# Kernel tuning notes

Hardware: AMD Instinct MI355X
Metric: run time of the kernel (lower is better)

Reference implementation:

```python
import jax, jax.numpy as jnp
import numpy as np
from jax import lax

K = 35
PAD = K // 2  # 17

def _maxpool_same(x):
    # x: [B, H, W]; torch MaxPool2d pads with -inf, stride 1, same spatial size
    return lax.reduce_window(
        x, -jnp.inf, lax.max,
        window_dimensions=(1, K, K),
        window_strides=(1, 1, 1),
        padding=[(0, 0), (PAD, PAD), (PAD, PAD)],
    )

def setup_inputs() -> dict:
    key = jax.random.key(0)
    k1, k2 = jax.random.split(key)
    shape = (16, 3, 512, 512)
    restored = jax.random.uniform(k1, shape, dtype=jnp.float32)
    target = jax.random.uniform(k2, shape, dtype=jnp.float32)
    return {"restored": restored, "target": target}

def reference(restored, target):
    r = _maxpool_same(jnp.min(restored, axis=1))  # channel-min then 35x35 max
    t = _maxpool_same(jnp.min(target, axis=1))
    out = jnp.mean(jnp.abs(r - t))
    return jax.nn.sigmoid(out)
```

## Files before the change

### kernel.cpp

```cpp
#include <hip/hip_runtime.h>
#include <math.h>

#define WID 512
#define HEI 512
#define NB  16
#define HW  ((size_t)HEI * WID)
#define NEG_INF (-INFINITY)

__global__ __launch_bounds__(256) void hmax_kernel(
    const float* __restrict__ rin, const float* __restrict__ tin,
    float* __restrict__ ws)
{
    const int h = blockIdx.x;
    const int z = blockIdx.y;
    const int b = z & 15;
    const float* __restrict__ in = (z < NB) ? rin : tin;
    const float* __restrict__ p  = in + (size_t)b * 3 * HW + (size_t)h * WID;

    __shared__ float sm[548];
    __shared__ float gm[137];

    const int tid = threadIdx.x;

    for (int i = tid; i < 548; i += 256) {
        int w = i - 17;
        float v = NEG_INF;
        if (w >= 0 && w < WID) {
            float a0 = __builtin_nontemporal_load(p + w);
            float a1 = __builtin_nontemporal_load(p + HW + w);
            float a2 = __builtin_nontemporal_load(p + 2 * HW + w);
            v = fminf(fminf(a0, a1), a2);
        }
        sm[i] = v;
    }
    __syncthreads();

    for (int g = tid; g < 137; g += 256) {
        gm[g] = fmaxf(fmaxf(sm[4*g], sm[4*g+1]), fmaxf(sm[4*g+2], sm[4*g+3]));
    }
    __syncthreads();

    float* __restrict__ wp = ws + (size_t)z * HW + (size_t)h * WID;
    #pragma unroll
    for (int rep = 0; rep < 2; ++rep) {
        const int a  = tid + rep * 256;
        const int bb = a + 34;
        const int j0 = (a + 3) >> 2;
        float m = fmaxf(fmaxf(sm[a], sm[a+1]), sm[a+2]);
        m = fmaxf(m, fmaxf(fmaxf(sm[bb], sm[bb-1]), sm[bb-2]));
        #pragma unroll
        for (int j = 0; j < 8; ++j) m = fmaxf(m, gm[j0 + j]);
        wp[a] = m;
    }
}

__global__ __launch_bounds__(256) void vmax_kernel(
    const float* __restrict__ rh, const float* __restrict__ th,
    float* __restrict__ acc)
{
    __shared__ float sm[100][64];
    __shared__ float gm[25][64];
    __shared__ float red[256];

    const int tid = threadIdx.x;
    const int col = tid & 63;
    const int ty  = tid >> 6;
    const int w0  = blockIdx.x * 64;
    const int h0  = blockIdx.y * 64;
    const int b   = blockIdx.z;

    float rtv[16];
    float tsum = 0.0f;

    #pragma unroll
    for (int tensor = 0; tensor < 2; ++tensor) {
        const float* __restrict__ pb =
            ((tensor == 0) ? rh : th) + (size_t)b * HW;

        for (int i = tid; i < 100 * 64; i += 256) {
            int row = i >> 6;
            int c   = i & 63;
            int hh  = h0 - 17 + row;
            float v = NEG_INF;
            if (row < 98 && hh >= 0 && hh < HEI)
                v = pb[(size_t)hh * WID + w0 + c];
            sm[row][c] = v;
        }
        __syncthreads();

        for (int i = tid; i < 25 * 64; i += 256) {
            int g = i >> 6;
            int c = i & 63;
            gm[g][c] = fmaxf(fmaxf(sm[4*g][c], sm[4*g+1][c]),
                             fmaxf(sm[4*g+2][c], sm[4*g+3][c]));
        }
        __syncthreads();

        #pragma unroll
        for (int k = 0; k < 16; ++k) {
            const int a  = ty * 16 + k;
            const int bb = a + 34;
            const int j0 = (a + 3) >> 2;
            float m = fmaxf(fmaxf(sm[a][col], sm[a+1][col]), sm[a+2][col]);
            m = fmaxf(m, fmaxf(fmaxf(sm[bb][col], sm[bb-1][col]), sm[bb-2][col]));
            #pragma unroll
            for (int j = 0; j < 8; ++j) m = fmaxf(m, gm[j0 + j][col]);
            if (tensor == 0) rtv[k] = m;
            else             tsum += fabsf(rtv[k] - m);
        }
        __syncthreads();
    }

    red[tid] = tsum;
    __syncthreads();
    for (int s = 128; s > 0; s >>= 1) {
        if (tid < s) red[tid] += red[tid + s];
        __syncthreads();
    }
    if (tid == 0) atomicAdd(acc, red[0]);
}

__global__ void finalize_kernel(const float* __restrict__ acc,
                                float* __restrict__ out)
{
    float s = acc[0] / 4194304.0f;
    out[0] = 1.0f / (1.0f + expf(-s));
}

extern "C" void kernel_launch(void* const* d_in, const int* in_sizes, int n_in,
                              void* d_out, int out_size, void* d_ws, size_t ws_size,
                              hipStream_t stream) {
    const float* rin = (const float*)d_in[0];
    const float* tin = (const float*)d_in[1];
    float* out = (float*)d_out;

    float* wsf = (float*)d_ws;
    float* rh  = wsf;
    float* th  = wsf + (size_t)NB * HW;
    float* acc = wsf + (size_t)2 * NB * HW;

    hipMemsetAsync(acc, 0, sizeof(float), stream);

    dim3 gA(HEI, 2 * NB);
    hipLaunchKernelGGL(hmax_kernel, gA, dim3(256), 0, stream, rin, tin, wsf);

    dim3 gB(WID / 64, HEI / 64, NB);
    hipLaunchKernelGGL(vmax_kernel, gB, dim3(256), 0, stream, rh, th, acc);

    hipLaunchKernelGGL(finalize_kernel, dim3(1), dim3(1), 0, stream, acc, out);
}
```

Measured before the change: 158.4 us.

## Vectorize max-pool passes, compute window maxes in registers, fuse finalize into reduction

The horizontal pass now handles two rows per block with float4 loads and stores. Each thread builds four outputs from shared block maxima held in registers, replacing the separate group-max shared array and its barrier. The vertical pass loads tiles as float4, keeps a 50-row column strip in registers and shares partial maxima across four outputs. The block reduction uses wave shuffles instead of a shared-memory tree. The memset and finalize launch are removed: the accumulator is zeroed inside the first kernel and the last block, found by an atomic ticket, computes the sigmoid. This cuts launch overhead, shared-memory traffic and sync points, at the cost of more register pressure and a reliance on kernel ordering for the in-kernel accumulator reset.

```diff
diff --git a/kernel.cpp b/kernel.cpp
--- a/kernel.cpp
+++ b/kernel.cpp
@@ -7,61 +7,68 @@
 #define HW  ((size_t)HEI * WID)
 #define NEG_INF (-INFINITY)
 
+typedef float f4 __attribute__((ext_vector_type(4)));
+
 __global__ __launch_bounds__(256) void hmax_kernel(
     const float* __restrict__ rin, const float* __restrict__ tin,
-    float* __restrict__ ws)
+    float* __restrict__ ws, float* __restrict__ acc)
 {
-    const int h = blockIdx.x;
-    const int z = blockIdx.y;
-    const int b = z & 15;
+    __shared__ float sm[2][552];
+    const int tid = threadIdx.x;
+    const int row = tid >> 7;
+    const int t   = tid & 127;
+    const int h   = blockIdx.x * 2 + row;
+    const int z   = blockIdx.y;
+    const int b   = z & 15;
     const float* __restrict__ in = (z < NB) ? rin : tin;
-    const float* __restrict__ p  = in + (size_t)b * 3 * HW + (size_t)h * WID;
 
-    __shared__ float sm[548];
-    __shared__ float gm[137];
+    if (blockIdx.x == 0 && blockIdx.y == 0 && tid < 2) acc[tid] = 0.0f;
 
-    const int tid = threadIdx.x;
+    if (tid < 80) {
+        int r2 = tid / 40, j = tid % 40;
+        sm[r2][(j < 20) ? j : (j + 512)] = NEG_INF;
+    }
 
-    for (int i = tid; i < 548; i += 256) {
-        int w = i - 17;
-        float v = NEG_INF;
-        if (w >= 0 && w < WID) {
-            float a0 = __builtin_nontemporal_load(p + w);
-            float a1 = __builtin_nontemporal_load(p + HW + w);
-            float a2 = __builtin_nontemporal_load(p + 2 * HW + w);
-            v = fminf(fminf(a0, a1), a2);
-        }
-        sm[i] = v;
-    }
+    const float* __restrict__ p = in + (size_t)b * 3 * HW + (size_t)h * WID;
+    f4 a0 = __builtin_nontemporal_load((const f4*)p + t);
+    f4 a1 = __builtin_nontemporal_load((const f4*)(p + HW) + t);
+    f4 a2 = __builtin_nontemporal_load((const f4*)(p + 2 * HW) + t);
+    f4 v;
+    v.x = fminf(fminf(a0.x, a1.x), a2.x);
+    v.y = fminf(fminf(a0.y, a1.y), a2.y);
+    v.z = fminf(fminf(a0.z, a1.z), a2.z);
+    v.w = fminf(fminf(a0.w, a1.w), a2.w);
+    *(f4*)&sm[row][20 + 4 * t] = v;
     __syncthreads();
 
-    for (int g = tid; g < 137; g += 256) {
-        gm[g] = fmaxf(fmaxf(sm[4*g], sm[4*g+1]), fmaxf(sm[4*g+2], sm[4*g+3]));
-    }
-    __syncthreads();
-
-    float* __restrict__ wp = ws + (size_t)z * HW + (size_t)h * WID;
+    const f4* __restrict__ smr = (const f4*)sm[row];
+    f4 vv[11];
     #pragma unroll
-    for (int rep = 0; rep < 2; ++rep) {
-        const int a  = tid + rep * 256;
-        const int bb = a + 34;
-        const int j0 = (a + 3) >> 2;
-        float m = fmaxf(fmaxf(sm[a], sm[a+1]), sm[a+2]);
-        m = fmaxf(m, fmaxf(fmaxf(sm[bb], sm[bb-1]), sm[bb-2]));
-        #pragma unroll
-        for (int j = 0; j < 8; ++j) m = fmaxf(m, gm[j0 + j]);
-        wp[a] = m;
-    }
+    for (int i = 0; i < 11; ++i) vv[i] = smr[t + i];
+    float q[10];
+    #pragma unroll
+    for (int i = 1; i <= 9; ++i)
+        q[i] = fmaxf(fmaxf(vv[i].x, vv[i].y), fmaxf(vv[i].z, vv[i].w));
+    float Q28 = fmaxf(fmaxf(fmaxf(q[2], q[3]), fmaxf(q[4], q[5])),
+                      fmaxf(fmaxf(q[6], q[7]), q[8]));
+    float Q18 = fmaxf(Q28, q[1]);
+    float Q29 = fmaxf(Q28, q[9]);
+    float s01 = fmaxf(vv[9].x, vv[9].y);
+    float s23 = fmaxf(vv[1].z, vv[1].w);
+    f4 o;
+    o.x = fmaxf(fmaxf(Q18, vv[0].w), s01);
+    o.y = fmaxf(Q18, fmaxf(s01, vv[9].z));
+    o.z = fmaxf(fmaxf(Q29, vv[1].y), s23);
+    o.w = fmaxf(Q29, fmaxf(s23, vv[10].x));
+    *((f4*)(ws + (size_t)z * HW + (size_t)h * WID) + t) = o;
 }
 
 __global__ __launch_bounds__(256) void vmax_kernel(
-    const float* __restrict__ rh, const float* __restrict__ th,
-    float* __restrict__ acc)
+    const float* __restrict__ ws, float* __restrict__ acc,
+    float* __restrict__ out)
 {
-    __shared__ float sm[100][64];
-    __shared__ float gm[25][64];
-    __shared__ float red[256];
-
+    __shared__ float sm[98][64];
+    __shared__ float red[4];
     const int tid = threadIdx.x;
     const int col = tid & 63;
     const int ty  = tid >> 6;
@@ -74,57 +81,63 @@
 
     #pragma unroll
     for (int tensor = 0; tensor < 2; ++tensor) {
-        const float* __restrict__ pb =
-            ((tensor == 0) ? rh : th) + (size_t)b * HW;
-
-        for (int i = tid; i < 100 * 64; i += 256) {
-            int row = i >> 6;
-            int c   = i & 63;
-            int hh  = h0 - 17 + row;
-            float v = NEG_INF;
-            if (row < 98 && hh >= 0 && hh < HEI)
-                v = pb[(size_t)hh * WID + w0 + c];
-            sm[row][c] = v;
+        const float* __restrict__ pb = ws + (size_t)(tensor * NB + b) * HW;
+        #pragma unroll
+        for (int i0 = 0; i0 < 1568; i0 += 256) {
+            int i = i0 + tid;
+            if (i < 1568) {
+                int r = i >> 4, c4 = i & 15;
+                int hh = h0 - 17 + r;
+                f4 v = {NEG_INF, NEG_INF, NEG_INF, NEG_INF};
+                if (hh >= 0 && hh < HEI)
+                    v = ((const f4*)pb)[hh * 128 + (w0 >> 2) + c4];
+                *(f4*)&sm[r][c4 * 4] = v;
+            }
         }
         __syncthreads();
 
-        for (int i = tid; i < 25 * 64; i += 256) {
-            int g = i >> 6;
-            int c = i & 63;
-            gm[g][c] = fmaxf(fmaxf(sm[4*g][c], sm[4*g+1][c]),
-                             fmaxf(sm[4*g+2][c], sm[4*g+3][c]));
-        }
-        __syncthreads();
-
+        float vc[50];
         #pragma unroll
-        for (int k = 0; k < 16; ++k) {
-            const int a  = ty * 16 + k;
-            const int bb = a + 34;
-            const int j0 = (a + 3) >> 2;
-            float m = fmaxf(fmaxf(sm[a][col], sm[a+1][col]), sm[a+2][col]);
-            m = fmaxf(m, fmaxf(fmaxf(sm[bb][col], sm[bb-1][col]), sm[bb-2][col]));
-            #pragma unroll
-            for (int j = 0; j < 8; ++j) m = fmaxf(m, gm[j0 + j][col]);
-            if (tensor == 0) rtv[k] = m;
-            else             tsum += fabsf(rtv[k] - m);
+        for (int i = 0; i < 50; ++i) vc[i] = sm[ty * 16 + i][col];
+        float q[12];
+        #pragma unroll
+        for (int i = 0; i < 12; ++i)
+            q[i] = fmaxf(fmaxf(vc[4*i], vc[4*i+1]), fmaxf(vc[4*i+2], vc[4*i+3]));
+        #pragma unroll
+        for (int m = 0; m < 4; ++m) {
+            float Qc = fmaxf(fmaxf(fmaxf(q[m+1], q[m+2]), fmaxf(q[m+3], q[m+4])),
+                             fmaxf(fmaxf(q[m+5], q[m+6]), q[m+7]));
+            float A  = fmaxf(Qc, q[m+8]);
+            float o0 = fmaxf(fmaxf(Qc, q[m]),
+                             fmaxf(fmaxf(vc[4*m+32], vc[4*m+33]), vc[4*m+34]));
+            float o1 = fmaxf(A, fmaxf(fmaxf(vc[4*m+1], vc[4*m+2]), vc[4*m+3]));
+            float o2 = fmaxf(A, fmaxf(fmaxf(vc[4*m+2], vc[4*m+3]), vc[4*m+36]));
+            float o3 = fmaxf(A, fmaxf(fmaxf(vc[4*m+3], vc[4*m+36]), vc[4*m+37]));
+            if (tensor == 0) {
+                rtv[4*m] = o0; rtv[4*m+1] = o1; rtv[4*m+2] = o2; rtv[4*m+3] = o3;
+            } else {
+                tsum += fabsf(rtv[4*m]   - o0) + fabsf(rtv[4*m+1] - o1)
+                      + fabsf(rtv[4*m+2] - o2) + fabsf(rtv[4*m+3] - o3);
+            }
         }
         __syncthreads();
     }
 
-    red[tid] = tsum;
+    #pragma unroll
+    for (int off = 32; off > 0; off >>= 1)
+        tsum += __shfl_down(tsum, off, 64);
+    if ((tid & 63) == 0) red[ty] = tsum;
     __syncthreads();
-    for (int s = 128; s > 0; s >>= 1) {
-        if (tid < s) red[tid] += red[tid + s];
-        __syncthreads();
+    if (tid == 0) {
+        float blocksum = red[0] + red[1] + red[2] + red[3];
+        atomicAdd(acc, blocksum);
+        __threadfence();
+        unsigned tk = atomicAdd((unsigned*)(acc + 1), 1u);
+        if (tk == 1023u) {
+            float s = atomicAdd(acc, 0.0f);
+            out[0] = 1.0f / (1.0f + expf(-s / 4194304.0f));
+        }
     }
-    if (tid == 0) atomicAdd(acc, red[0]);
-}
-
-__global__ void finalize_kernel(const float* __restrict__ acc,
-                                float* __restrict__ out)
-{
-    float s = acc[0] / 4194304.0f;
-    out[0] = 1.0f / (1.0f + expf(-s));
 }
 
 extern "C" void kernel_launch(void* const* d_in, const int* in_sizes, int n_in,
@@ -135,17 +148,11 @@
     float* out = (float*)d_out;
 
     float* wsf = (float*)d_ws;
-    float* rh  = wsf;
-    float* th  = wsf + (size_t)NB * HW;
     float* acc = wsf + (size_t)2 * NB * HW;
 
-    hipMemsetAsync(acc, 0, sizeof(float), stream);
-
-    dim3 gA(HEI, 2 * NB);
-    hipLaunchKernelGGL(hmax_kernel, gA, dim3(256), 0, stream, rin, tin, wsf);
+    dim3 gA(HEI / 2, 2 * NB);
+    hipLaunchKernelGGL(hmax_kernel, gA, dim3(256), 0, stream, rin, tin, wsf, acc);
 
     dim3 gB(WID / 64, HEI / 64, NB);
-    hipLaunchKernelGGL(vmax_kernel, gB, dim3(256), 0, stream, rh, th, acc);
-
-    hipLaunchKernelGGL(finalize_kernel, dim3(1), dim3(1), 0, stream, acc, out);
+    hipLaunchKernelGGL(vmax_kernel, gB, dim3(256), 0, stream, wsf, acc, out);
 }
```

New measurement: 154.0 us. 1.03x faster.
